# Kernel tuning notes

Hardware: AMD Instinct MI355X
Metric: run time of the kernel (lower is better)

## Reference

```python
import jax, jax.numpy as jnp
import numpy as np
import math

BATCH, TBINS, SPATIAL = 16, 8, 16
WIN, SHIFT = 8, 4
DIM, HEADS = 1024, 16
HD = DIM // HEADS
N = WIN * WIN          # tokens per window = 64
NW = (SPATIAL // WIN) ** 2  # windows per image = 4
HIDDEN = 4 * DIM


def _static_buffers():
    ws = WIN
    # continuous relative coords table (signed log-spaced), [(2ws-1)^2, 2]
    c = np.arange(-(ws - 1), ws, dtype=np.float32) / (ws - 1)
    c = np.sign(c) * np.log2(1.0 + np.abs(c))
    gh, gw = np.meshgrid(c, c, indexing='ij')
    table = np.stack([gh, gw], axis=-1).reshape(-1, 2).astype(np.float32)
    # relative position index, [N, N]
    coords = np.stack(np.meshgrid(np.arange(ws), np.arange(ws), indexing='ij')).reshape(2, -1)
    rel = (coords[:, :, None] - coords[:, None, :]).transpose(1, 2, 0)
    rel[..., 0] += ws - 1
    rel[..., 1] += ws - 1
    rel[..., 0] *= 2 * ws - 1
    rp_idx = rel.sum(-1)  # [N, N] int
    # shifted-window attention mask, [NW, N, N]
    img = np.zeros((SPATIAL, SPATIAL), dtype=np.float32)
    slices = [slice(0, -ws), slice(-ws, -SHIFT), slice(-SHIFT, None)]
    cnt = 0
    for hs in slices:
        for wsl in slices:
            img[hs, wsl] = cnt
            cnt += 1
    mw = img.reshape(SPATIAL // ws, ws, SPATIAL // ws, ws).transpose(0, 2, 1, 3).reshape(-1, ws * ws)
    diff = mw[:, None, :] - mw[:, :, None]  # matches unsqueeze(1) - unsqueeze(2)
    attn_mask = np.where(diff != 0, np.float32(-100.0), np.float32(0.0))
    return jnp.asarray(table), jnp.asarray(rp_idx), jnp.asarray(attn_mask)

CPB_TABLE, RP_IDX, ATTN_MASK = _static_buffers()


def _window_partition(x):  # [B, H, W, C] -> [B*nW, ws, ws, C]
    b, h, w, c = x.shape
    x = x.reshape(b, h // WIN, WIN, w // WIN, WIN, c).transpose(0, 1, 3, 2, 4, 5)
    return x.reshape(-1, WIN, WIN, c)


def _window_reverse(win, h, w):  # [B*nW, ws, ws, C] -> [B, H, W, C]
    b = win.shape[0] // ((h // WIN) * (w // WIN))
    x = win.reshape(b, h // WIN, w // WIN, WIN, WIN, -1).transpose(0, 1, 3, 2, 4, 5)
    return x.reshape(b, h, w, -1)


def _layernorm(x, g, b):
    m = jnp.mean(x, -1, keepdims=True)
    v = jnp.mean((x - m) ** 2, -1, keepdims=True)
    return (x - m) * jax.lax.rsqrt(v + 1e-5) * g + b


def _l2norm(x):
    return x / jnp.maximum(jnp.linalg.norm(x, axis=-1, keepdims=True), 1e-12)


def setup_inputs() -> dict:
    key = jax.random.key(0)
    ks = jax.random.split(key, 16)
    s = 0.02
    inp = {
        'x': jax.random.normal(ks[0], (BATCH, TBINS * SPATIAL * SPATIAL, DIM), jnp.float32),
        'qkv_w': jax.random.normal(ks[1], (3 * DIM, DIM), jnp.float32) * s,
        'q_bias': jnp.zeros((DIM,), jnp.float32),
        'v_bias': jnp.zeros((DIM,), jnp.float32),
        'logit_scale': jnp.full((HEADS, 1, 1), math.log(10.0), jnp.float32),
        'cpb_w1': jax.random.normal(ks[2], (512, 2), jnp.float32) * s,
        'cpb_b1': jnp.zeros((512,), jnp.float32),
        'cpb_w2': jax.random.normal(ks[3], (HEADS, 512), jnp.float32) * s,
        'proj_w': jax.random.normal(ks[4], (DIM, DIM), jnp.float32) * s,
        'proj_b': jnp.zeros((DIM,), jnp.float32),
        'norm1_w': jnp.ones((DIM,), jnp.float32),
        'norm1_b': jnp.zeros((DIM,), jnp.float32),
        'fc1_w': jax.random.normal(ks[5], (HIDDEN, DIM), jnp.float32) * s,
        'fc1_b': jnp.zeros((HIDDEN,), jnp.float32),
        'fc2_w': jax.random.normal(ks[6], (DIM, HIDDEN), jnp.float32) * s,
        'fc2_b': jnp.zeros((DIM,), jnp.float32),
        'norm2_w': jnp.ones((DIM,), jnp.float32),
        'norm2_b': jnp.zeros((DIM,), jnp.float32),
    }
    return inp


def reference(x, qkv_w, q_bias, v_bias, logit_scale, cpb_w1, cpb_b1, cpb_w2,
              proj_w, proj_b, norm1_w, norm1_b, fc1_w, fc1_b, fc2_w, fc2_b,
              norm2_w, norm2_b):
    B, L, C = x.shape
    xs = x.reshape(B * TBINS, SPATIAL, SPATIAL, C)
    shortcut = xs
    # cyclic shift
    shifted = jnp.roll(xs, shift=(-SHIFT, -SHIFT), axis=(1, 2))
    xw = _window_partition(shifted).reshape(-1, N, C)  # [Bw, N, C]
    Bw = xw.shape[0]

    # qkv with q/v bias only (no k bias)
    qkv_bias = jnp.concatenate([q_bias, jnp.zeros_like(v_bias), v_bias])
    qkv = xw @ qkv_w.T + qkv_bias
    qkv = qkv.reshape(Bw, N, 3, HEADS, HD).transpose(2, 0, 3, 1, 4)
    q, k, v = qkv[0], qkv[1], qkv[2]  # [Bw, h, N, hd]

    # cosine attention with clamped learnable logit scale
    attn = jnp.einsum('bhnd,bhmd->bhnm', _l2norm(q), _l2norm(k))
    scale = jnp.exp(jnp.minimum(logit_scale, math.log(100.0)))  # [h,1,1]
    attn = attn * scale[None]

    # continuous relative position bias via CPB-MLP
    tbl = jax.nn.relu(CPB_TABLE @ cpb_w1.T + cpb_b1) @ cpb_w2.T  # [(2ws-1)^2, h]
    tbl = 16.0 * jax.nn.sigmoid(tbl)
    bias = tbl[RP_IDX.reshape(-1)].reshape(N, N, HEADS).transpose(2, 0, 1)  # [h,N,N]
    attn = attn + bias[None]

    # shift mask
    attn = attn.reshape(Bw // NW, NW, HEADS, N, N) + ATTN_MASK[None, :, None]
    attn = attn.reshape(Bw, HEADS, N, N)
    attn = jax.nn.softmax(attn, axis=-1)

    out = jnp.einsum('bhnm,bhmd->bhnd', attn, v)
    out = out.transpose(0, 2, 1, 3).reshape(Bw, N, C)
    out = out @ proj_w.T + proj_b

    out = _window_reverse(out.reshape(-1, WIN, WIN, C), SPATIAL, SPATIAL)
    out = jnp.roll(out, shift=(SHIFT, SHIFT), axis=(1, 2))

    # SwinV2 post-norm residuals
    xs = shortcut + _layernorm(out, norm1_w, norm1_b)
    h = jax.nn.gelu(xs @ fc1_w.T + fc1_b, approximate=False) @ fc2_w.T + fc2_b
    xs = xs + _layernorm(h, norm2_w, norm2_b)
    return xs.reshape(B, L, C)
```

## Files before the change

kernel.cpp:

```cpp
#include <hip/hip_runtime.h>
#include <hip/hip_bf16.h>
#include <math.h>

typedef __hip_bfloat16 bf16;
typedef __attribute__((ext_vector_type(8))) short short8;
typedef __attribute__((ext_vector_type(4))) short short4v;
typedef __attribute__((ext_vector_type(4))) float floatx4;
typedef __attribute__((ext_vector_type(2))) unsigned int uint2v;

#define DEV static __device__ __forceinline__

DEV float bf2f(unsigned short u) {
  union { unsigned int i; float f; } x;
  x.i = ((unsigned int)u) << 16;
  return x.f;
}
DEV unsigned short f2bf_bits(float f) {
  union { bf16 h; unsigned short u; } x;
  x.h = __float2bfloat16(f);
  return x.u;
}
DEV short8 cvt8(float4 a, float4 b) {
  short8 r;
  r[0] = (short)f2bf_bits(a.x); r[1] = (short)f2bf_bits(a.y);
  r[2] = (short)f2bf_bits(a.z); r[3] = (short)f2bf_bits(a.w);
  r[4] = (short)f2bf_bits(b.x); r[5] = (short)f2bf_bits(b.y);
  r[6] = (short)f2bf_bits(b.z); r[7] = (short)f2bf_bits(b.w);
  return r;
}

DEV float gelu_fast(float v) {
  float y = v * (1.5957691216f + 0.0713548163f * v * v);
  return __fdividef(v, 1.f + __expf(-y));
}

DEV void gload_lds16(const unsigned short* g, unsigned short* l) {
  __builtin_amdgcn_global_load_lds((const __attribute__((address_space(1))) void*)g,
                                   (__attribute__((address_space(3))) void*)l,
                                   16, 0, 0);
}

DEV int gather_win_row(int wr) {
  int bw = wr >> 6, n = wr & 63;
  int bt = bw >> 2, w2 = bw & 3;
  int wi = w2 >> 1, wj = w2 & 1;
  int r = n >> 3, c = n & 7;
  int sr = (wi * 8 + r + 4) & 15;
  int sc = (wj * 8 + c + 4) & 15;
  return bt * 256 + sr * 16 + sc;
}

enum { BIAS_SIMPLE = 0, BIAS_QKV = 1 };
enum { ACT_NONE = 0, ACT_GELU = 1 };

__global__ __launch_bounds__(256) void cvt_bf16(const float* __restrict__ in,
                                                bf16* __restrict__ out, int n) {
  int i = (blockIdx.x * 256 + threadIdx.x) * 8;
  if (i >= n) return;
  float4 a = *reinterpret_cast<const float4*>(in + i);
  float4 b = *reinterpret_cast<const float4*>(in + i + 4);
  *reinterpret_cast<short8*>((unsigned short*)out + i) = cvt8(a, b);
}

template <int GATHER, int BIASMODE, int ACT>
__global__ __launch_bounds__(256, 2) void gemm_bt(
    const unsigned short* __restrict__ A, const unsigned short* __restrict__ B,
    const float* __restrict__ bias0, const float* __restrict__ bias1,
    bf16* __restrict__ C, int M, int N, int K)
{
  __shared__ __align__(16) unsigned short sh[128 * 136];
  unsigned short* As = sh;
  unsigned short* Bs = sh + 8192;

  const int tid = threadIdx.x;
  const int lane = tid & 63;
  const int wave = tid >> 6;
  const int waveM = wave >> 1, waveN = wave & 1;
  const int tileM = blockIdx.x * 128, tileN = blockIdx.y * 128;

  const int row0 = tid >> 3;
  const int kOff = (tid & 7) * 8;

  const unsigned short* ag[4];
  const unsigned short* bg[4];
  unsigned short* al[4];
  unsigned short* bl[4];
#pragma unroll
  for (int t = 0; t < 4; ++t) {
    int gr = tileM + row0 + 32 * t;
    int sr = GATHER ? gather_win_row(gr) : gr;
    ag[t] = A + (size_t)sr * (size_t)K + (size_t)kOff;
    bg[t] = B + (size_t)(tileN + row0 + 32 * t) * (size_t)K + (size_t)kOff;
    al[t] = &As[(row0 + 32 * t) * 64 + kOff];
    bl[t] = &Bs[(row0 + 32 * t) * 64 + kOff];
  }

  floatx4 acc[4][4];
#pragma unroll
  for (int i = 0; i < 4; ++i)
#pragma unroll
    for (int j = 0; j < 4; ++j) acc[i][j] = (floatx4){0.f, 0.f, 0.f, 0.f};

  for (int k0 = 0; k0 < K; k0 += 64) {
#pragma unroll
    for (int t = 0; t < 4; ++t) {
      gload_lds16(ag[t] + k0, al[t]);
      gload_lds16(bg[t] + k0, bl[t]);
    }
    __syncthreads();
#pragma unroll
    for (int ks = 0; ks < 2; ++ks) {
      const int kk = ks * 32 + (lane >> 4) * 8;
      short8 af[4], bfv[4];
#pragma unroll
      for (int i = 0; i < 4; ++i)
        af[i] = *reinterpret_cast<const short8*>(
            &As[(waveM * 64 + i * 16 + (lane & 15)) * 64 + kk]);
#pragma unroll
      for (int j = 0; j < 4; ++j)
        bfv[j] = *reinterpret_cast<const short8*>(
            &Bs[(waveN * 64 + j * 16 + (lane & 15)) * 64 + kk]);
#pragma unroll
      for (int i = 0; i < 4; ++i)
#pragma unroll
        for (int j = 0; j < 4; ++j)
          acc[i][j] = __builtin_amdgcn_mfma_f32_16x16x32_bf16(af[i], bfv[j], acc[i][j], 0, 0, 0);
    }
    __syncthreads();
  }

#pragma unroll
  for (int j = 0; j < 4; ++j) {
    const int colL = waveN * 64 + j * 16 + (lane & 15);
    const int colG = tileN + colL;
    float bv;
    if (BIASMODE == BIAS_QKV) {
      if (colG < 1024) bv = bias0[colG];
      else if (colG < 2048) bv = 0.f;
      else bv = bias1[colG - 2048];
    } else {
      bv = bias0[colG];
    }
#pragma unroll
    for (int i = 0; i < 4; ++i) {
      const int rL = waveM * 64 + i * 16 + ((lane >> 4) * 4);
#pragma unroll
      for (int r = 0; r < 4; ++r) {
        float v = acc[i][j][r] + bv;
        if (ACT == ACT_GELU) v = gelu_fast(v);
        sh[(rL + r) * 136 + colL] = f2bf_bits(v);
      }
    }
  }
  __syncthreads();
  {
    const int rowR = tid >> 4;
    const int colR = (tid & 15) * 8;
#pragma unroll
    for (int s = 0; s < 8; ++s) {
      const int row = s * 16 + rowR;
      uint4 val = *reinterpret_cast<const uint4*>(&sh[row * 136 + colR]);
      *reinterpret_cast<uint4*>(
          (unsigned short*)C + (size_t)(tileM + row) * (size_t)N + tileN + colR) = val;
    }
  }
}

__global__ __launch_bounds__(512) void cpb_kernel(
    const float* __restrict__ w1, const float* __restrict__ b1,
    const float* __restrict__ w2, float* __restrict__ TBL)
{
  __shared__ float hid[512];
  const int i = blockIdx.x;
  const int j = threadIdx.x;
  const float d0 = ((float)(i / 15) - 7.f) / 7.f;
  const float d1 = ((float)(i % 15) - 7.f) / 7.f;
  const float t0 = copysignf(log2f(1.f + fabsf(d0)), d0);
  const float t1 = copysignf(log2f(1.f + fabsf(d1)), d1);
  float hv = t0 * w1[j * 2] + t1 * w1[j * 2 + 1] + b1[j];
  hid[j] = fmaxf(hv, 0.f);
  __syncthreads();
  if (j < 16) {
    float s = 0.f;
    for (int jj = 0; jj < 512; ++jj) s += w2[j * 512 + jj] * hid[jj];
    TBL[j * 225 + i] = 16.f / (1.f + expf(-s));
  }
}

__global__ __launch_bounds__(256) void attn_mfma(
    const bf16* __restrict__ QKV, const float* __restrict__ TBL,
    const float* __restrict__ ls, bf16* __restrict__ ATT)
{
  __shared__ __align__(16) unsigned short Ps[4][64][72];
  __shared__ float tbs[4][226];
  __shared__ int ids[64];

  const int tid = threadIdx.x;
  const int w = tid >> 6;
  const int l = tid & 63;
  const int q = l & 15;
  const int g = l >> 4;
  const int bw = blockIdx.x >> 2;
  const int h = (blockIdx.x & 3) * 4 + w;

  const unsigned short* qkvu = (const unsigned short*)QKV;
  const size_t rbase = (size_t)(bw * 64) * 3072;

  if (tid < 64) {
    const int w2 = bw & 3, wi = w2 >> 1, wj = w2 & 1;
    const int r = tid >> 3, c = tid & 7;
    const int rr = (wi == 0) ? 0 : (r < 4 ? 1 : 2);
    const int rc = (wj == 0) ? 0 : (c < 4 ? 1 : 2);
    ids[tid] = rr * 3 + rc;
  }
#pragma unroll
  for (int i = 0; i < 4; ++i) {
    int idx = i * 64 + l;
    if (idx < 225) tbs[w][idx] = TBL[h * 225 + idx];
  }
  __syncthreads();

  short8 kf[4][2], qf[4][2];
#pragma unroll
  for (int i = 0; i < 4; ++i) {
    const unsigned short* rp = qkvu + rbase + (size_t)(16 * i + q) * 3072 + h * 64 + g * 8;
    qf[i][0] = *reinterpret_cast<const short8*>(rp);
    qf[i][1] = *reinterpret_cast<const short8*>(rp + 32);
    kf[i][0] = *reinterpret_cast<const short8*>(rp + 1024);
    kf[i][1] = *reinterpret_cast<const short8*>(rp + 1024 + 32);
  }

  float rk4[4], rq4[4];
#pragma unroll
  for (int i = 0; i < 4; ++i) {
    float sk = 0.f, sq = 0.f;
#pragma unroll
    for (int ks = 0; ks < 2; ++ks)
#pragma unroll
      for (int e = 0; e < 8; ++e) {
        float kv = bf2f((unsigned short)kf[i][ks][e]);
        float qv = bf2f((unsigned short)qf[i][ks][e]);
        sk += kv * kv; sq += qv * qv;
      }
    sk += __shfl_xor(sk, 16); sk += __shfl_xor(sk, 32);
    sq += __shfl_xor(sq, 16); sq += __shfl_xor(sq, 32);
    rk4[i] = 1.f / fmaxf(sqrtf(sk), 1e-12f);
    rq4[i] = 1.f / fmaxf(sqrtf(sq), 1e-12f);
  }
  const float scl = expf(fminf(ls[h], 4.60517019f));
  float rqs[4];
#pragma unroll
  for (int j = 0; j < 4; ++j) rqs[j] = rq4[j] * scl;

  floatx4 acc[4][4];
#pragma unroll
  for (int i = 0; i < 4; ++i)
#pragma unroll
    for (int j = 0; j < 4; ++j) acc[i][j] = (floatx4){0.f, 0.f, 0.f, 0.f};
#pragma unroll
  for (int ks = 0; ks < 2; ++ks)
#pragma unroll
    for (int i = 0; i < 4; ++i)
#pragma unroll
      for (int j = 0; j < 4; ++j)
        acc[i][j] = __builtin_amdgcn_mfma_f32_16x16x32_bf16(kf[i][ks], qf[j][ks], acc[i][j], 0, 0, 0);

  short8 vf[4][2];
  const unsigned short* vbase = qkvu + rbase + 2048 + h * 64;
#pragma unroll
  for (int jp = 0; jp < 4; ++jp)
#pragma unroll
    for (int ks = 0; ks < 2; ++ks) {
      const int m0 = ks * 32 + g * 8;
      const unsigned short* vp = vbase + 16 * jp + q;
      union { short8 v; unsigned short u[8]; } pk;
#pragma unroll
      for (int e = 0; e < 8; ++e)
        pk.u[e] = vp[(size_t)(m0 + e) * 3072];
      vf[jp][ks] = pk.v;
    }

  int idn[4], rtn[4], ctn[4];
#pragma unroll
  for (int j = 0; j < 4; ++j) {
    const int n = 16 * j + q;
    rtn[j] = n >> 3; ctn[j] = n & 7; idn[j] = ids[n];
  }
#pragma unroll
  for (int i = 0; i < 4; ++i) {
#pragma unroll
    for (int r = 0; r < 4; ++r) {
      const int m = 16 * i + 4 * g + r;
      const float rkm = __shfl(rk4[i], 4 * g + r);
      const int rm = m >> 3, cm = m & 7;
      const int idm = ids[m];
#pragma unroll
      for (int j = 0; j < 4; ++j) {
        float v = acc[i][j][r] * (rkm * rqs[j]) +
                  tbs[w][(rtn[j] - rm + 7) * 15 + (ctn[j] - cm + 7)];
        if (idm != idn[j]) v -= 100.f;
        acc[i][j][r] = v;
      }
    }
  }

  float rs4[4];
#pragma unroll
  for (int j = 0; j < 4; ++j) {
    float mx = acc[0][j][0];
#pragma unroll
    for (int i = 0; i < 4; ++i)
#pragma unroll
      for (int r = 0; r < 4; ++r) mx = fmaxf(mx, acc[i][j][r]);
    mx = fmaxf(mx, __shfl_xor(mx, 16));
    mx = fmaxf(mx, __shfl_xor(mx, 32));
    float sm = 0.f;
#pragma unroll
    for (int i = 0; i < 4; ++i)
#pragma unroll
      for (int r = 0; r < 4; ++r) {
        float e = __expf(acc[i][j][r] - mx);
        acc[i][j][r] = e; sm += e;
      }
    sm += __shfl_xor(sm, 16);
    sm += __shfl_xor(sm, 32);
    rs4[j] = 1.f / sm;
  }

#pragma unroll
  for (int j = 0; j < 4; ++j)
#pragma unroll
    for (int i = 0; i < 4; ++i) {
      uint2v pw;
      pw[0] = (unsigned int)f2bf_bits(acc[i][j][0]) |
              ((unsigned int)f2bf_bits(acc[i][j][1]) << 16);
      pw[1] = (unsigned int)f2bf_bits(acc[i][j][2]) |
              ((unsigned int)f2bf_bits(acc[i][j][3]) << 16);
      *reinterpret_cast<uint2v*>(&Ps[w][16 * j + q][16 * i + 4 * g]) = pw;
    }

  floatx4 o[4][4];
#pragma unroll
  for (int i = 0; i < 4; ++i)
#pragma unroll
    for (int j = 0; j < 4; ++j) o[i][j] = (floatx4){0.f, 0.f, 0.f, 0.f};
#pragma unroll
  for (int ks = 0; ks < 2; ++ks) {
    short8 pa[4];
#pragma unroll
    for (int i2 = 0; i2 < 4; ++i2)
      pa[i2] = *reinterpret_cast<const short8*>(&Ps[w][16 * i2 + q][ks * 32 + g * 8]);
#pragma unroll
    for (int i2 = 0; i2 < 4; ++i2)
#pragma unroll
      for (int j2 = 0; j2 < 4; ++j2)
        o[i2][j2] = __builtin_amdgcn_mfma_f32_16x16x32_bf16(pa[i2], vf[j2][ks], o[i2][j2], 0, 0, 0);
  }

  unsigned short* op = (unsigned short*)ATT + (size_t)(bw * 64) * 1024 + h * 64;
#pragma unroll
  for (int i2 = 0; i2 < 4; ++i2)
#pragma unroll
    for (int r = 0; r < 4; ++r) {
      const float rsn = __shfl(rs4[i2], 4 * g + r);
      const int row = 16 * i2 + 4 * g + r;
#pragma unroll
      for (int j2 = 0; j2 < 4; ++j2)
        op[(size_t)row * 1024 + 16 * j2 + q] = f2bf_bits(o[i2][j2][r] * rsn);
    }
}

template <bool GATHER, bool WB>
__global__ __launch_bounds__(256) void ln_residual(
    const bf16* __restrict__ src, const float* base,
    const float* __restrict__ gw, const float* __restrict__ gb,
    float* out, bf16* __restrict__ out_bf)
{
  const int tok = blockIdx.x * 4 + (threadIdx.x >> 6);
  const int lane = threadIdx.x & 63;
  int srow;
  if (GATHER) {
    const int bt = tok >> 8, rem = tok & 255, i = rem >> 4, j = rem & 15;
    const int p = (i + 12) & 15, qq = (j + 12) & 15;
    srow = (bt * 4 + (p >> 3) * 2 + (qq >> 3)) * 64 + (p & 7) * 8 + (qq & 7);
  } else {
    srow = tok;
  }
  const unsigned short* sp = (const unsigned short*)src + (size_t)srow * 1024 + lane * 16;
  short8 lv0 = *reinterpret_cast<const short8*>(sp);
  short8 lv1 = *reinterpret_cast<const short8*>(sp + 8);
  float v[16];
  float s = 0.f, sq = 0.f;
#pragma unroll
  for (int u = 0; u < 8; ++u) {
    float f = bf2f((unsigned short)lv0[u]); v[u] = f; s += f; sq += f * f;
    float g = bf2f((unsigned short)lv1[u]); v[u + 8] = g; s += g; sq += g * g;
  }
#pragma unroll
  for (int off = 32; off > 0; off >>= 1) { s += __shfl_xor(s, off); sq += __shfl_xor(sq, off); }
  const float mean = s * (1.f / 1024.f);
  const float var = sq * (1.f / 1024.f) - mean * mean;
  const float rstd = rsqrtf(var + 1e-5f);

  const float* bp = base + (size_t)tok * 1024 + lane * 16;
  float* op = out + (size_t)tok * 1024 + lane * 16;
  unsigned short* obp = WB ? ((unsigned short*)out_bf + (size_t)tok * 1024 + lane * 16) : nullptr;
  union { short8 v; unsigned short u[8]; } ob0, ob1;
#pragma unroll
  for (int q4 = 0; q4 < 4; ++q4) {
    float4 b4 = *reinterpret_cast<const float4*>(bp + q4 * 4);
    float bl[4] = {b4.x, b4.y, b4.z, b4.w};
    float4 o4;
    float* ol = (float*)&o4;
#pragma unroll
    for (int u = 0; u < 4; ++u) {
      const int c = lane * 16 + q4 * 4 + u;
      ol[u] = bl[u] + (v[q4 * 4 + u] - mean) * rstd * gw[c] + gb[c];
      if (WB) {
        if (q4 < 2) ob0.u[q4 * 4 + u] = f2bf_bits(ol[u]);
        else ob1.u[(q4 - 2) * 4 + u] = f2bf_bits(ol[u]);
      }
    }
    *reinterpret_cast<float4*>(op + q4 * 4) = o4;
  }
  if (WB) {
    *reinterpret_cast<short8*>(obp) = ob0.v;
    *reinterpret_cast<short8*>(obp + 8) = ob1.v;
  }
}

extern "C" void kernel_launch(void* const* d_in, const int* in_sizes, int n_in,
                              void* d_out, int out_size, void* d_ws, size_t ws_size,
                              hipStream_t stream) {
  (void)in_sizes; (void)n_in; (void)out_size;
  const float* x      = (const float*)d_in[0];
  const float* qkv_w  = (const float*)d_in[1];
  const float* q_bias = (const float*)d_in[2];
  const float* v_bias = (const float*)d_in[3];
  const float* lscale = (const float*)d_in[4];
  const float* cpb_w1 = (const float*)d_in[5];
  const float* cpb_b1 = (const float*)d_in[6];
  const float* cpb_w2 = (const float*)d_in[7];
  const float* proj_w = (const float*)d_in[8];
  const float* proj_b = (const float*)d_in[9];
  const float* n1w    = (const float*)d_in[10];
  const float* n1b    = (const float*)d_in[11];
  const float* fc1_w  = (const float*)d_in[12];
  const float* fc1_b  = (const float*)d_in[13];
  const float* fc2_w  = (const float*)d_in[14];
  const float* fc2_b  = (const float*)d_in[15];
  const float* n2w    = (const float*)d_in[16];
  const float* n2b    = (const float*)d_in[17];
  float* out = (float*)d_out;

  char* ws = (char*)d_ws;
  bf16*  QKV  = (bf16*)(ws);
  bf16*  H    = (bf16*)(ws);
  bf16*  ATT  = (bf16*)(ws + 67108864);
  bf16*  XSB  = (bf16*)(ws + 67108864);
  bf16*  F2   = (bf16*)(ws + 67108864);
  bf16*  XBF  = (bf16*)(ws + 83886080);
  bf16*  PROJ = (bf16*)(ws + 83886080);
  float* TBL  = (float*)(ws + 100663296);

  const bool persist = ws_size >= (size_t)125845504;
  bf16* WQKV, *WPROJ, *WF1, *WF2;
  if (persist) {
    WQKV  = (bf16*)(ws + 100679680);
    WPROJ = (bf16*)(ws + 106971136);
    WF1   = (bf16*)(ws + 109068288);
    WF2   = (bf16*)(ws + 117456896);
  } else {
    WQKV  = (bf16*)(ws + 67108864);
    WPROJ = (bf16*)(ws + 50331648);
    WF1   = (bf16*)(ws + 83886080);
    WF2   = (bf16*)(ws + 83886080 + 8388608);
  }

  cpb_kernel<<<225, 512, 0, stream>>>(cpb_w1, cpb_b1, cpb_w2, TBL);
  if (persist) {
    cvt_bf16<<<1536, 256, 0, stream>>>(qkv_w, WQKV, 3145728);
    cvt_bf16<<<512, 256, 0, stream>>>(proj_w, WPROJ, 1048576);
    cvt_bf16<<<2048, 256, 0, stream>>>(fc1_w, WF1, 4194304);
    cvt_bf16<<<2048, 256, 0, stream>>>(fc2_w, WF2, 4194304);
  }

  for (int ch = 0; ch < 4; ++ch) {
    const size_t tokBase = (size_t)ch * 8192;
    const float* x_c = x + tokBase * 1024;
    float* out_c = out + tokBase * 1024;

    cvt_bf16<<<4096, 256, 0, stream>>>(x_c, XBF, 8388608);
    if (!persist) {
      cvt_bf16<<<1536, 256, 0, stream>>>(qkv_w, WQKV, 3145728);
      cvt_bf16<<<512, 256, 0, stream>>>(proj_w, WPROJ, 1048576);
    }

    gemm_bt<1, BIAS_QKV, ACT_NONE><<<dim3(64, 24), 256, 0, stream>>>(
        (const unsigned short*)XBF, (const unsigned short*)WQKV,
        q_bias, v_bias, QKV, 8192, 3072, 1024);
    attn_mfma<<<512, 256, 0, stream>>>(QKV, TBL, lscale, ATT);
    gemm_bt<0, BIAS_SIMPLE, ACT_NONE><<<dim3(64, 8), 256, 0, stream>>>(
        (const unsigned short*)ATT, (const unsigned short*)WPROJ,
        proj_b, nullptr, PROJ, 8192, 1024, 1024);
    ln_residual<true, true><<<2048, 256, 0, stream>>>(PROJ, x_c, n1w, n1b, out_c, XSB);
    if (!persist) {
      cvt_bf16<<<2048, 256, 0, stream>>>(fc1_w, WF1, 4194304);
      cvt_bf16<<<2048, 256, 0, stream>>>(fc2_w, WF2, 4194304);
    }
    gemm_bt<0, BIAS_SIMPLE, ACT_GELU><<<dim3(64, 32), 256, 0, stream>>>(
        (const unsigned short*)XSB, (const unsigned short*)WF1,
        fc1_b, nullptr, H, 8192, 4096, 1024);
    gemm_bt<0, BIAS_SIMPLE, ACT_NONE><<<dim3(64, 8), 256, 0, stream>>>(
        (const unsigned short*)H, (const unsigned short*)WF2,
        fc2_b, nullptr, F2, 8192, 1024, 4096);
    ln_residual<false, false><<<2048, 256, 0, stream>>>(F2, out_c, n2w, n2b, out_c, nullptr);
  }
}
```

Baseline: 1.660 ms.

## Add 256x256 double-buffered 8-wave GEMM with LDS-staged epilogue

Adds a new GEMM kernel with 256x256 tiles, 512 threads (8 waves) and 128KB dynamic LDS, double-buffered in K halves. Global-to-LDS loads for the next K tile are interleaved with MFMA consumption using vmcnt waits, barriers and s_setprio. It also remaps workgroup IDs in groups of 8 and writes the bf16 output through LDS so global stores are coalesced. All four transformer GEMMs use it when the shared-memory attribute can be set, falling back to the old kernel otherwise. Risks include lower occupancy from the large LDS footprint, fewer blocks (128 for the proj/fc2 GEMMs, under a full wave on a 256-CU part) and fine-grained barrier overhead.

```diff
diff --git a/kernel.cpp b/kernel.cpp
--- a/kernel.cpp
+++ b/kernel.cpp
@@ -60,6 +60,145 @@
   float4 a = *reinterpret_cast<const float4*>(in + i);
   float4 b = *reinterpret_cast<const float4*>(in + i + 4);
   *reinterpret_cast<short8*>((unsigned short*)out + i) = cvt8(a, b);
+}
+
+#define VMCNT(N_) asm volatile("s_waitcnt vmcnt(" #N_ ")" ::: "memory")
+#define BARRIER() do { __builtin_amdgcn_s_barrier(); asm volatile("" ::: "memory"); } while (0)
+
+#define STG(BUF, ISB, KS, KT) do { \
+    char* dst_ = smem + (BUF) * 65536 + (ISB) * 32768 + (KS) * 16384; \
+    gload_lds16(((ISB) ? bgp[0] : agp[0]) + (KT) * 64 + (KS) * 32, \
+                (unsigned short*)(dst_ + soff0)); \
+    gload_lds16(((ISB) ? bgp[1] : agp[1]) + (KT) * 64 + (KS) * 32, \
+                (unsigned short*)(dst_ + soff1)); \
+  } while (0)
+
+#define CONSUME(KS, IH, DO_B) do { \
+    const char* ac_ = smem + bsel * 65536 + (KS) * 16384; \
+    if (DO_B) { \
+      const char* bc_ = ac_ + 32768; \
+      _Pragma("unroll") \
+      for (int j_ = 0; j_ < 4; ++j_) \
+        bfr[j_] = *reinterpret_cast<const short8*>(bc_ + bBase + j_ * 1024); \
+    } \
+    _Pragma("unroll") \
+    for (int i_ = 0; i_ < 4; ++i_) \
+      af[i_] = *reinterpret_cast<const short8*>(ac_ + aBase + ((IH) * 4 + i_) * 1024); \
+    __builtin_amdgcn_s_setprio(1); \
+    _Pragma("unroll") \
+    for (int i_ = 0; i_ < 4; ++i_) \
+      _Pragma("unroll") \
+      for (int j_ = 0; j_ < 4; ++j_) \
+        acc[(IH) * 4 + i_][j_] = __builtin_amdgcn_mfma_f32_16x16x32_bf16( \
+            af[i_], bfr[j_], acc[(IH) * 4 + i_][j_], 0, 0, 0); \
+    __builtin_amdgcn_s_setprio(0); \
+  } while (0)
+
+template <int GATHER, int BIASMODE, int ACT>
+__global__ __launch_bounds__(512, 2) void gemm8p(
+    const unsigned short* __restrict__ A, const unsigned short* __restrict__ B,
+    const float* __restrict__ bias0, const float* __restrict__ bias1,
+    bf16* __restrict__ C, int M, int N, int K)
+{
+  extern __shared__ __align__(16) char smem[];
+  const int tid = threadIdx.x;
+  const int lane = tid & 63;
+  const int wave = tid >> 6;
+  const int wm = wave >> 2, wn = wave & 3;
+
+  const int gx = gridDim.x;
+  const int nwg = gx * gridDim.y;
+  int lin = blockIdx.y * gx + blockIdx.x;
+  if ((nwg & 7) == 0) lin = (lin & 7) * (nwg >> 3) + (lin >> 3);
+  const int tileM = (lin % gx) * 256;
+  const int tileN = (lin / gx) * 256;
+
+  const unsigned short* agp[2];
+  const unsigned short* bgp[2];
+#pragma unroll
+  for (int u = 0; u < 2; ++u) {
+    int s = u * 512 + tid;
+    int row = s >> 2, slot = s & 3;
+    int gr = tileM + row;
+    int sr = GATHER ? gather_win_row(gr) : gr;
+    agp[u] = A + (size_t)sr * (size_t)K + slot * 8;
+    bgp[u] = B + (size_t)(tileN + row) * (size_t)K + slot * 8;
+  }
+  const int soff0 = tid * 16;
+  const int soff1 = (512 + tid) * 16;
+
+  const int aBase = (wm * 128 + (lane & 15)) * 64 + (lane >> 4) * 16;
+  const int bBase = (wn * 64 + (lane & 15)) * 64 + (lane >> 4) * 16;
+
+  floatx4 acc[8][4];
+#pragma unroll
+  for (int i = 0; i < 8; ++i)
+#pragma unroll
+    for (int j = 0; j < 4; ++j) acc[i][j] = (floatx4){0.f, 0.f, 0.f, 0.f};
+
+  short8 af[4], bfr[4];
+  const int NT = K >> 6;
+  int bsel = 0;
+
+  STG(0, 0, 0, 0); STG(0, 1, 0, 0); STG(0, 0, 1, 0); STG(0, 1, 1, 0);
+  VMCNT(0);
+  BARRIER();
+
+  for (int t = 0; t < NT - 1; ++t) {
+    const int nb = bsel ^ 1;
+    const int kt1 = t + 1;
+    STG(nb, 0, 0, kt1); VMCNT(6); BARRIER(); CONSUME(0, 0, 1);
+    STG(nb, 1, 0, kt1); VMCNT(6); BARRIER(); CONSUME(0, 1, 0);
+    STG(nb, 0, 1, kt1); VMCNT(6); BARRIER(); CONSUME(1, 0, 1);
+    STG(nb, 1, 1, kt1); VMCNT(6); BARRIER(); CONSUME(1, 1, 0);
+    bsel = nb;
+  }
+  VMCNT(4); BARRIER();
+  CONSUME(0, 0, 1);
+  CONSUME(0, 1, 0);
+  VMCNT(0); BARRIER();
+  CONSUME(1, 0, 1);
+  CONSUME(1, 1, 0);
+
+  __syncthreads();
+  unsigned short* sh16 = (unsigned short*)smem;
+  const int g = lane >> 4, q = lane & 15;
+  float bv[4];
+#pragma unroll
+  for (int j = 0; j < 4; ++j) {
+    const int colG = tileN + wn * 64 + j * 16 + q;
+    if (BIASMODE == BIAS_QKV) {
+      bv[j] = (colG < 1024) ? bias0[colG] : (colG < 2048 ? 0.f : bias1[colG - 2048]);
+    } else {
+      bv[j] = bias0[colG];
+    }
+  }
+#pragma unroll
+  for (int h = 0; h < 2; ++h) {
+    if (wm == h) {
+#pragma unroll
+      for (int i = 0; i < 8; ++i)
+#pragma unroll
+        for (int j = 0; j < 4; ++j)
+#pragma unroll
+          for (int r = 0; r < 4; ++r) {
+            float v = acc[i][j][r] + bv[j];
+            if (ACT == ACT_GELU) v = gelu_fast(v);
+            sh16[(i * 16 + g * 4 + r) * 264 + wn * 64 + j * 16 + q] = f2bf_bits(v);
+          }
+    }
+    __syncthreads();
+#pragma unroll
+    for (int pass = 0; pass < 8; ++pass) {
+      const int idx = pass * 512 + tid;
+      const int row = idx >> 5, c16 = idx & 31;
+      uint4 val = *reinterpret_cast<const uint4*>(&sh16[row * 264 + c16 * 8]);
+      *reinterpret_cast<uint4*>(
+          (unsigned short*)C + (size_t)(tileM + h * 128 + row) * (size_t)N +
+          tileN + c16 * 8) = val;
+    }
+    __syncthreads();
+  }
 }
 
 template <int GATHER, int BIASMODE, int ACT>
@@ -111,10 +250,10 @@
 #pragma unroll
     for (int ks = 0; ks < 2; ++ks) {
       const int kk = ks * 32 + (lane >> 4) * 8;
-      short8 af[4], bfv[4];
+      short8 afv[4], bfv[4];
 #pragma unroll
       for (int i = 0; i < 4; ++i)
-        af[i] = *reinterpret_cast<const short8*>(
+        afv[i] = *reinterpret_cast<const short8*>(
             &As[(waveM * 64 + i * 16 + (lane & 15)) * 64 + kk]);
 #pragma unroll
       for (int j = 0; j < 4; ++j)
@@ -124,7 +263,7 @@
       for (int i = 0; i < 4; ++i)
 #pragma unroll
         for (int j = 0; j < 4; ++j)
-          acc[i][j] = __builtin_amdgcn_mfma_f32_16x16x32_bf16(af[i], bfv[j], acc[i][j], 0, 0, 0);
+          acc[i][j] = __builtin_amdgcn_mfma_f32_16x16x32_bf16(afv[i], bfv[j], acc[i][j], 0, 0, 0);
     }
     __syncthreads();
   }
@@ -453,6 +592,20 @@
   const float* n2b    = (const float*)d_in[17];
   float* out = (float*)d_out;
 
+  static int attr_ok = -1;
+  if (attr_ok < 0) {
+    hipError_t e1 = hipFuncSetAttribute(
+        reinterpret_cast<const void*>(&gemm8p<1, BIAS_QKV, ACT_NONE>),
+        hipFuncAttributeMaxDynamicSharedMemorySize, 131072);
+    hipError_t e2 = hipFuncSetAttribute(
+        reinterpret_cast<const void*>(&gemm8p<0, BIAS_SIMPLE, ACT_NONE>),
+        hipFuncAttributeMaxDynamicSharedMemorySize, 131072);
+    hipError_t e3 = hipFuncSetAttribute(
+        reinterpret_cast<const void*>(&gemm8p<0, BIAS_SIMPLE, ACT_GELU>),
+        hipFuncAttributeMaxDynamicSharedMemorySize, 131072);
+    attr_ok = (e1 == hipSuccess && e2 == hipSuccess && e3 == hipSuccess) ? 1 : 0;
+  }
+
   char* ws = (char*)d_ws;
   bf16*  QKV  = (bf16*)(ws);
   bf16*  H    = (bf16*)(ws);
@@ -496,24 +649,45 @@
       cvt_bf16<<<512, 256, 0, stream>>>(proj_w, WPROJ, 1048576);
     }
 
-    gemm_bt<1, BIAS_QKV, ACT_NONE><<<dim3(64, 24), 256, 0, stream>>>(
-        (const unsigned short*)XBF, (const unsigned short*)WQKV,
-        q_bias, v_bias, QKV, 8192, 3072, 1024);
+    if (attr_ok) {
+      gemm8p<1, BIAS_QKV, ACT_NONE><<<dim3(32, 12), 512, 131072, stream>>>(
+          (const unsigned short*)XBF, (const unsigned short*)WQKV,
+          q_bias, v_bias, QKV, 8192, 3072, 1024);
+    } else {
+      gemm_bt<1, BIAS_QKV, ACT_NONE><<<dim3(64, 24), 256, 0, stream>>>(
+          (const unsigned short*)XBF, (const unsigned short*)WQKV,
+          q_bias, v_bias, QKV, 8192, 3072, 1024);
+    }
     attn_mfma<<<512, 256, 0, stream>>>(QKV, TBL, lscale, ATT);
-    gemm_bt<0, BIAS_SIMPLE, ACT_NONE><<<dim3(64, 8), 256, 0, stream>>>(
-        (const unsigned short*)ATT, (const unsigned short*)WPROJ,
-        proj_b, nullptr, PROJ, 8192, 1024, 1024);
+    if (attr_ok) {
+      gemm8p<0, BIAS_SIMPLE, ACT_NONE><<<dim3(32, 4), 512, 131072, stream>>>(
+          (const unsigned short*)ATT, (const unsigned short*)WPROJ,
+          proj_b, nullptr, PROJ, 8192, 1024, 1024);
+    } else {
+      gemm_bt<0, BIAS_SIMPLE, ACT_NONE><<<dim3(64, 8), 256, 0, stream>>>(
+          (const unsigned short*)ATT, (const unsigned short*)WPROJ,
+          proj_b, nullptr, PROJ, 8192, 1024, 1024);
+    }
     ln_residual<true, true><<<2048, 256, 0, stream>>>(PROJ, x_c, n1w, n1b, out_c, XSB);
     if (!persist) {
       cvt_bf16<<<2048, 256, 0, stream>>>(fc1_w, WF1, 4194304);
       cvt_bf16<<<2048, 256, 0, stream>>>(fc2_w, WF2, 4194304);
     }
-    gemm_bt<0, BIAS_SIMPLE, ACT_GELU><<<dim3(64, 32), 256, 0, stream>>>(
-        (const unsigned short*)XSB, (const unsigned short*)WF1,
-        fc1_b, nullptr, H, 8192, 4096, 1024);
-    gemm_bt<0, BIAS_SIMPLE, ACT_NONE><<<dim3(64, 8), 256, 0, stream>>>(
-        (const unsigned short*)H, (const unsigned short*)WF2,
-        fc2_b, nullptr, F2, 8192, 1024, 4096);
+    if (attr_ok) {
+      gemm8p<0, BIAS_SIMPLE, ACT_GELU><<<dim3(32, 16), 512, 131072, stream>>>(
+          (const unsigned short*)XSB, (const unsigned short*)WF1,
+          fc1_b, nullptr, H, 8192, 4096, 1024);
+      gemm8p<0, BIAS_SIMPLE, ACT_NONE><<<dim3(32, 4), 512, 131072, stream>>>(
+          (const unsigned short*)H, (const unsigned short*)WF2,
+          fc2_b, nullptr, F2, 8192, 1024, 4096);
+    } else {
+      gemm_bt<0, BIAS_SIMPLE, ACT_GELU><<<dim3(64, 32), 256, 0, stream>>>(
+          (const unsigned short*)XSB, (const unsigned short*)WF1,
+          fc1_b, nullptr, H, 8192, 4096, 1024);
+      gemm_bt<0, BIAS_SIMPLE, ACT_NONE><<<dim3(64, 8), 256, 0, stream>>>(
+          (const unsigned short*)H, (const unsigned short*)WF2,
+          fc2_b, nullptr, F2, 8192, 1024, 4096);
+    }
     ln_residual<false, false><<<2048, 256, 0, stream>>>(F2, out_c, n2w, n2b, out_c, nullptr);
   }
 }
```

New measurement: 1.725 ms. 3.9% more time.
